# Kernel optimization log

Hardware: AMD Instinct MI355X
Metric: run time of the kernel (lower is better)

The kernel has to match this reference:

```python
import jax, jax.numpy as jnp
import numpy as np

N_NODES = 10000
N_EDGES = 160000
IN_DIM = 512
HID = 128
OUT = 64


def setup_inputs() -> dict:
    key = jax.random.key(0)
    ks = jax.random.split(key, 8)
    x = jax.random.normal(ks[0], (N_NODES, IN_DIM), dtype=jnp.float32)
    edge_index = jax.random.randint(ks[1], (2, N_EDGES), 0, N_NODES, dtype=jnp.int32)
    s = 0.02
    return {
        "x": x,
        "edge_index": edge_index,
        "W1_l": jax.random.normal(ks[2], (HID, IN_DIM), dtype=jnp.float32) * s,
        "W1_r": jax.random.normal(ks[3], (HID, IN_DIM), dtype=jnp.float32) * s,
        "b1": jnp.zeros((HID,), dtype=jnp.float32),
        "W2_l": jax.random.normal(ks[4], (OUT, HID), dtype=jnp.float32) * s,
        "W2_r": jax.random.normal(ks[5], (OUT, HID), dtype=jnp.float32) * s,
        "b2": jnp.zeros((OUT,), dtype=jnp.float32),
    }


def _sage_conv(x, src, dst, W_l, W_r, b, n_nodes):
    # PyG SAGEConv (aggr='mean', root_weight=True):
    #   out = lin_l(mean over incoming edges of x[src]) + lin_r(x)
    msg = x[src]  # [E, d] gather
    agg = jax.ops.segment_sum(msg, dst, num_segments=n_nodes)  # [N, d]
    cnt = jax.ops.segment_sum(jnp.ones_like(dst, dtype=x.dtype), dst, num_segments=n_nodes)
    agg = agg / jnp.maximum(cnt, 1.0)[:, None]  # mean with empty-node guard
    return agg @ W_l.T + x @ W_r.T + b


def reference(x, edge_index, W1_l, W1_r, b1, W2_l, W2_r, b2):
    src, dst = edge_index[0], edge_index[1]
    n = x.shape[0]
    h = _sage_conv(x, src, dst, W1_l, W1_r, b1, n)
    h = jax.nn.relu(h)
    z = _sage_conv(h, src, dst, W2_l, W2_r, b2, n)
    return z
```

## Files before the change

kernel.cpp:

```cpp
#include <hip/hip_runtime.h>

#define N_NODES 10000
#define N_EDGES 160000
#define IN_DIM 512
#define HID 128
#define OUT_DIM 64
#define CAP 64

typedef __attribute__((ext_vector_type(8))) short bf16x8;
typedef __attribute__((ext_vector_type(4))) float f32x4;

__device__ inline ushort f2b(float f) {
    unsigned u = __float_as_uint(f);
    u += 0x7fff + ((u >> 16) & 1);
    return (ushort)(u >> 16);
}
__device__ inline uint pack2(float a, float b) {
    return (uint)f2b(a) | ((uint)f2b(b) << 16);
}
__device__ inline float blo(uint u) { return __uint_as_float(u << 16); }
__device__ inline float bhi(uint u) { return __uint_as_float(u & 0xffff0000u); }

__global__ void zero_deg(int* __restrict__ deg) {
    int i = blockIdx.x * blockDim.x + threadIdx.x;
    if (i < N_NODES / 4) ((int4*)deg)[i] = make_int4(0, 0, 0, 0);
}

__device__ __forceinline__ void gemm1_body(int n0, int by,
    const float* __restrict__ A, const float* __restrict__ bpanel,
    ushort* __restrict__ XL, float* __restrict__ XR) {
    __shared__ __align__(16) ushort Asm[32 * 64];
    __shared__ __align__(16) ushort Bsm[64 * 64];

    const int t    = threadIdx.x;
    const int lane = t & 63;
    const int w    = t >> 6;
    const int wr   = w & 1;
    const int wc   = w >> 1;
    const int m0   = by * 32;
    const int kch  = lane >> 4;
    const int lrow = lane & 15;

    f32x4 acc[2] = {};

    for (int k0 = 0; k0 < IN_DIM; k0 += 64) {
        {
            int row = t >> 3, c = t & 7;
            int m = m0 + row;
            uint4 o = make_uint4(0u, 0u, 0u, 0u);
            if (m < N_NODES) {
                const float* p = A + (size_t)m * IN_DIM + k0 + c * 8;
                float4 v0 = reinterpret_cast<const float4*>(p)[0];
                float4 v1 = reinterpret_cast<const float4*>(p)[1];
                o.x = pack2(v0.x, v0.y); o.y = pack2(v0.z, v0.w);
                o.z = pack2(v1.x, v1.y); o.w = pack2(v1.z, v1.w);
            }
            *reinterpret_cast<uint4*>(&Asm[row * 64 + ((c ^ (row & 7)) << 3)]) = o;
        }
        #pragma unroll
        for (int ch = t; ch < 64 * 8; ch += 256) {
            int row = ch >> 3, c = ch & 7;
            const float* p = bpanel + (size_t)row * IN_DIM + k0 + c * 8;
            float4 v0 = reinterpret_cast<const float4*>(p)[0];
            float4 v1 = reinterpret_cast<const float4*>(p)[1];
            uint4 o;
            o.x = pack2(v0.x, v0.y); o.y = pack2(v0.z, v0.w);
            o.z = pack2(v1.x, v1.y); o.w = pack2(v1.z, v1.w);
            *reinterpret_cast<uint4*>(&Bsm[row * 64 + ((c ^ (row & 7)) << 3)]) = o;
        }
        __syncthreads();

        const int arow = wr * 16 + lrow;
        #pragma unroll
        for (int h = 0; h < 2; ++h) {
            int c = h * 4 + kch;
            bf16x8 afr = *reinterpret_cast<const bf16x8*>(&Asm[arow * 64 + ((c ^ (arow & 7)) << 3)]);
            #pragma unroll
            for (int cf = 0; cf < 2; ++cf) {
                int brow = wc * 32 + cf * 16 + lrow;
                bf16x8 bfr = *reinterpret_cast<const bf16x8*>(&Bsm[brow * 64 + ((c ^ (brow & 7)) << 3)]);
                acc[cf] = __builtin_amdgcn_mfma_f32_16x16x32_bf16(afr, bfr, acc[cf], 0, 0, 0);
            }
        }
        __syncthreads();
    }

    #pragma unroll
    for (int cf = 0; cf < 2; ++cf) {
        int col = n0 + wc * 32 + cf * 16 + lrow;
        #pragma unroll
        for (int j = 0; j < 4; ++j) {
            int row = m0 + wr * 16 + kch * 4 + j;
            if (row >= N_NODES) continue;
            if (col < HID) XL[(size_t)row * HID + col] = f2b(acc[cf][j]);
            else           XR[(size_t)row * HID + (col - HID)] = acc[cf][j];
        }
    }
}

#define ROWB ((N_NODES + 31) / 32)
#define G1_BLOCKS (4 * ROWB)
#define FILL_BLOCKS ((N_EDGES + 255) / 256)

__global__ __launch_bounds__(256) void fat_gemm1_fill(
    const float* __restrict__ x,
    const float* __restrict__ w1l, const float* __restrict__ w1r,
    ushort* __restrict__ XL, float* __restrict__ XR,
    const int* __restrict__ src, const int* __restrict__ dst,
    int* __restrict__ deg, int* __restrict__ bell) {
    int b = blockIdx.x;
    if (b < G1_BLOCKS) {
        int bx = b / ROWB, by = b % ROWB;
        const float* bpanel = (bx < 2) ? (w1l + (size_t)bx * 64 * IN_DIM)
                                       : (w1r + (size_t)(bx - 2) * 64 * IN_DIM);
        gemm1_body(bx * 64, by, x, bpanel, XL, XR);
    } else {
        int e = (b - G1_BLOCKS) * 256 + threadIdx.x;
        if (e < N_EDGES) {
            int d = dst[e];
            int pos = atomicAdd(&deg[d], 1);
            if (pos < CAP) bell[d * CAP + pos] = src[e];
        }
    }
}

__global__ __launch_bounds__(512) void gather1_gemm2(
    const ushort* __restrict__ XL, const float* __restrict__ XR,
    const float* __restrict__ b1, const int* __restrict__ deg,
    const int* __restrict__ bell,
    const float* __restrict__ w2l, const float* __restrict__ w2r,
    ushort* __restrict__ HL, float* __restrict__ HR) {
    __shared__ __align__(16) ushort Ah[32 * 128];
    __shared__ __align__(16) ushort Bs[128 * 128];

    const int t    = threadIdx.x;
    const int lane = t & 63;
    const int w    = t >> 6;
    const int base = blockIdx.x * 32;

    #pragma unroll
    for (int ch = t; ch < 128 * 16; ch += 512) {
        int row = ch >> 4, c = ch & 15;
        const float* p = ((row < 64) ? (w2l + (size_t)row * HID)
                                     : (w2r + (size_t)(row - 64) * HID)) + c * 8;
        float4 v0 = reinterpret_cast<const float4*>(p)[0];
        float4 v1 = reinterpret_cast<const float4*>(p)[1];
        uint4 o;
        o.x = pack2(v0.x, v0.y); o.y = pack2(v0.z, v0.w);
        o.z = pack2(v1.x, v1.y); o.w = pack2(v1.z, v1.w);
        *reinterpret_cast<uint4*>(&Bs[row * 128 + ((c ^ (row & 7)) << 3)]) = o;
    }

    #pragma unroll
    for (int q = 0; q < 4; ++q) {
        int r = w * 4 + q;
        int n = base + r;
        float v0 = 0.f, v1 = 0.f;
        if (n < N_NODES) {
            int d = min(deg[n], CAP);
            const int* lst = bell + (size_t)n * CAP;
            float a0 = 0.f, a1 = 0.f;
            int i = 0;
            for (; i + 4 <= d; i += 4) {
                int s0 = lst[i], s1 = lst[i + 1], s2 = lst[i + 2], s3 = lst[i + 3];
                uint u0 = *(const uint*)(XL + (size_t)s0 * 128 + lane * 2);
                uint u1 = *(const uint*)(XL + (size_t)s1 * 128 + lane * 2);
                uint u2 = *(const uint*)(XL + (size_t)s2 * 128 + lane * 2);
                uint u3 = *(const uint*)(XL + (size_t)s3 * 128 + lane * 2);
                a0 += blo(u0) + blo(u1) + blo(u2) + blo(u3);
                a1 += bhi(u0) + bhi(u1) + bhi(u2) + bhi(u3);
            }
            for (; i < d; ++i) {
                uint u = *(const uint*)(XL + (size_t)lst[i] * 128 + lane * 2);
                a0 += blo(u); a1 += bhi(u);
            }
            float inv = (d > 0) ? (1.0f / (float)d) : 0.0f;
            float2 xv = *(const float2*)&XR[(size_t)n * 128 + lane * 2];
            v0 = fmaxf(a0 * inv + xv.x + b1[lane * 2], 0.f);
            v1 = fmaxf(a1 * inv + xv.y + b1[lane * 2 + 1], 0.f);
        }
        int c = lane >> 2;
        *(uint*)&Ah[r * 128 + ((c ^ (r & 7)) << 3) + (lane & 3) * 2] = pack2(v0, v1);
    }
    __syncthreads();

    const int wr = w & 1, cw = w >> 1;
    const int kch = lane >> 4, lrow = lane & 15;
    const int arow = wr * 16 + lrow;
    f32x4 acc[2] = {};
    #pragma unroll
    for (int ks = 0; ks < 4; ++ks) {
        int c = ks * 4 + kch;
        bf16x8 afr = *reinterpret_cast<const bf16x8*>(&Ah[arow * 128 + ((c ^ (arow & 7)) << 3)]);
        #pragma unroll
        for (int cf = 0; cf < 2; ++cf) {
            int brow = cw * 32 + cf * 16 + lrow;
            bf16x8 bfr = *reinterpret_cast<const bf16x8*>(&Bs[brow * 128 + ((c ^ (brow & 7)) << 3)]);
            acc[cf] = __builtin_amdgcn_mfma_f32_16x16x32_bf16(afr, bfr, acc[cf], 0, 0, 0);
        }
    }

    #pragma unroll
    for (int cf = 0; cf < 2; ++cf) {
        int col = cw * 32 + cf * 16 + lrow;
        #pragma unroll
        for (int j = 0; j < 4; ++j) {
            int row = base + wr * 16 + kch * 4 + j;
            if (row >= N_NODES) continue;
            if (col < OUT_DIM) HL[(size_t)row * OUT_DIM + col] = f2b(acc[cf][j]);
            else               HR[(size_t)row * OUT_DIM + (col - OUT_DIM)] = acc[cf][j];
        }
    }
}

__global__ __launch_bounds__(256) void gather2(
    const ushort* __restrict__ V, const float* __restrict__ xr,
    const float* __restrict__ b, const int* __restrict__ deg,
    const int* __restrict__ bell, float* __restrict__ out) {
    int wave = threadIdx.x >> 6;
    int lane = threadIdx.x & 63;
    int n = blockIdx.x * 4 + wave;
    if (n >= N_NODES) return;

    int d = min(deg[n], CAP);
    const int* lst = bell + (size_t)n * CAP;

    float a0 = 0.f;
    int i = 0;
    for (; i + 4 <= d; i += 4) {
        int s0 = lst[i], s1 = lst[i + 1], s2 = lst[i + 2], s3 = lst[i + 3];
        a0 += blo((uint)V[(size_t)s0 * 64 + lane]) + blo((uint)V[(size_t)s1 * 64 + lane])
            + blo((uint)V[(size_t)s2 * 64 + lane]) + blo((uint)V[(size_t)s3 * 64 + lane]);
    }
    for (; i < d; ++i) a0 += blo((uint)V[(size_t)lst[i] * 64 + lane]);

    float inv = (d > 0) ? (1.0f / (float)d) : 0.0f;
    out[(size_t)n * 64 + lane] = a0 * inv + xr[(size_t)n * 64 + lane] + b[lane];
}

extern "C" void kernel_launch(void* const* d_in, const int* in_sizes, int n_in,
                              void* d_out, int out_size, void* d_ws, size_t ws_size,
                              hipStream_t stream) {
    const float* x   = (const float*)d_in[0];
    const int*   ei  = (const int*)d_in[1];
    const int*   src = ei;
    const int*   dst = ei + N_EDGES;
    const float* W1l = (const float*)d_in[2];
    const float* W1r = (const float*)d_in[3];
    const float* b1  = (const float*)d_in[4];
    const float* W2l = (const float*)d_in[5];
    const float* W2r = (const float*)d_in[6];
    const float* b2  = (const float*)d_in[7];
    float*       out = (float*)d_out;

    int* deg  = (int*)d_ws;
    int* bell = deg + N_NODES;
    ushort* XL = (ushort*)(bell + (size_t)N_NODES * CAP);
    float*  XR = (float*)(XL + (size_t)N_NODES * HID);
    ushort* HL = (ushort*)(XR + (size_t)N_NODES * HID);
    float*  HR = (float*)(HL + (size_t)N_NODES * OUT_DIM);

    zero_deg<<<(N_NODES / 4 + 255) / 256, 256, 0, stream>>>(deg);

    fat_gemm1_fill<<<G1_BLOCKS + FILL_BLOCKS, 256, 0, stream>>>(
        x, W1l, W1r, XL, XR, src, dst, deg, bell);

    gather1_gemm2<<<ROWB, 512, 0, stream>>>(XL, XR, b1, deg, bell, W2l, W2r, HL, HR);

    gather2<<<(N_NODES + 3) / 4, 256, 0, stream>>>(HL, HR, b2, deg, bell, out);
}
```

Measured before the change: 68.94 us.

## Widen GEMM1 tiles, store root terms in bf16, shrink gather1 blocks

GEMM1 blocks now compute 128 output columns instead of 64, which halves the GEMM1 grid and the number of times each x tile is re-read and converted. The root-weight intermediates XR and HR are stored as bf16 instead of fp32, halving their write and read traffic. The gather1+GEMM2 kernel moves to 16-row blocks of 1024 threads with one node per wave and one MFMA column tile per wave, which gives more blocks for the gather. This adds bf16 rounding on the root path, and each of the smaller gather1 blocks reloads the full W2 panel.

```diff
diff --git a/kernel.cpp b/kernel.cpp
--- a/kernel.cpp
+++ b/kernel.cpp
@@ -26,11 +26,12 @@
     if (i < N_NODES / 4) ((int4*)deg)[i] = make_int4(0, 0, 0, 0);
 }
 
-__device__ __forceinline__ void gemm1_body(int n0, int by,
+__device__ __forceinline__ void gemm1_body(int bx, int by,
     const float* __restrict__ A, const float* __restrict__ bpanel,
-    ushort* __restrict__ XL, float* __restrict__ XR) {
+    ushort* __restrict__ XL, ushort* __restrict__ XR) {
+    constexpr int CF = 4;
     __shared__ __align__(16) ushort Asm[32 * 64];
-    __shared__ __align__(16) ushort Bsm[64 * 64];
+    __shared__ __align__(16) ushort Bsm[128 * 64];
 
     const int t    = threadIdx.x;
     const int lane = t & 63;
@@ -38,10 +39,11 @@
     const int wr   = w & 1;
     const int wc   = w >> 1;
     const int m0   = by * 32;
+    const int n0   = bx * 128;
     const int kch  = lane >> 4;
     const int lrow = lane & 15;
 
-    f32x4 acc[2] = {};
+    f32x4 acc[CF] = {};
 
     for (int k0 = 0; k0 < IN_DIM; k0 += 64) {
         {
@@ -58,7 +60,7 @@
             *reinterpret_cast<uint4*>(&Asm[row * 64 + ((c ^ (row & 7)) << 3)]) = o;
         }
         #pragma unroll
-        for (int ch = t; ch < 64 * 8; ch += 256) {
+        for (int ch = t; ch < 128 * 8; ch += 256) {
             int row = ch >> 3, c = ch & 7;
             const float* p = bpanel + (size_t)row * IN_DIM + k0 + c * 8;
             float4 v0 = reinterpret_cast<const float4*>(p)[0];
@@ -76,8 +78,8 @@
             int c = h * 4 + kch;
             bf16x8 afr = *reinterpret_cast<const bf16x8*>(&Asm[arow * 64 + ((c ^ (arow & 7)) << 3)]);
             #pragma unroll
-            for (int cf = 0; cf < 2; ++cf) {
-                int brow = wc * 32 + cf * 16 + lrow;
+            for (int cf = 0; cf < CF; ++cf) {
+                int brow = wc * 64 + cf * 16 + lrow;
                 bf16x8 bfr = *reinterpret_cast<const bf16x8*>(&Bsm[brow * 64 + ((c ^ (brow & 7)) << 3)]);
                 acc[cf] = __builtin_amdgcn_mfma_f32_16x16x32_bf16(afr, bfr, acc[cf], 0, 0, 0);
             }
@@ -86,34 +88,32 @@
     }
 
     #pragma unroll
-    for (int cf = 0; cf < 2; ++cf) {
-        int col = n0 + wc * 32 + cf * 16 + lrow;
+    for (int cf = 0; cf < CF; ++cf) {
+        int col = n0 + wc * 64 + cf * 16 + lrow;
         #pragma unroll
         for (int j = 0; j < 4; ++j) {
             int row = m0 + wr * 16 + kch * 4 + j;
             if (row >= N_NODES) continue;
             if (col < HID) XL[(size_t)row * HID + col] = f2b(acc[cf][j]);
-            else           XR[(size_t)row * HID + (col - HID)] = acc[cf][j];
+            else           XR[(size_t)row * HID + (col - HID)] = f2b(acc[cf][j]);
         }
     }
 }
 
 #define ROWB ((N_NODES + 31) / 32)
-#define G1_BLOCKS (4 * ROWB)
+#define G1_BLOCKS (2 * ROWB)
 #define FILL_BLOCKS ((N_EDGES + 255) / 256)
 
 __global__ __launch_bounds__(256) void fat_gemm1_fill(
     const float* __restrict__ x,
     const float* __restrict__ w1l, const float* __restrict__ w1r,
-    ushort* __restrict__ XL, float* __restrict__ XR,
+    ushort* __restrict__ XL, ushort* __restrict__ XR,
     const int* __restrict__ src, const int* __restrict__ dst,
     int* __restrict__ deg, int* __restrict__ bell) {
     int b = blockIdx.x;
     if (b < G1_BLOCKS) {
         int bx = b / ROWB, by = b % ROWB;
-        const float* bpanel = (bx < 2) ? (w1l + (size_t)bx * 64 * IN_DIM)
-                                       : (w1r + (size_t)(bx - 2) * 64 * IN_DIM);
-        gemm1_body(bx * 64, by, x, bpanel, XL, XR);
+        gemm1_body(bx, by, x, (bx == 0) ? w1l : w1r, XL, XR);
     } else {
         int e = (b - G1_BLOCKS) * 256 + threadIdx.x;
         if (e < N_EDGES) {
@@ -124,22 +124,22 @@
     }
 }
 
-__global__ __launch_bounds__(512) void gather1_gemm2(
-    const ushort* __restrict__ XL, const float* __restrict__ XR,
+__global__ __launch_bounds__(1024) void gather1_gemm2(
+    const ushort* __restrict__ XL, const ushort* __restrict__ XR,
     const float* __restrict__ b1, const int* __restrict__ deg,
     const int* __restrict__ bell,
     const float* __restrict__ w2l, const float* __restrict__ w2r,
-    ushort* __restrict__ HL, float* __restrict__ HR) {
-    __shared__ __align__(16) ushort Ah[32 * 128];
+    ushort* __restrict__ HL, ushort* __restrict__ HR) {
+    __shared__ __align__(16) ushort Ah[16 * 128];
     __shared__ __align__(16) ushort Bs[128 * 128];
 
     const int t    = threadIdx.x;
     const int lane = t & 63;
     const int w    = t >> 6;
-    const int base = blockIdx.x * 32;
+    const int base = blockIdx.x * 16;
 
     #pragma unroll
-    for (int ch = t; ch < 128 * 16; ch += 512) {
+    for (int ch = t; ch < 128 * 16; ch += 1024) {
         int row = ch >> 4, c = ch & 15;
         const float* p = ((row < 64) ? (w2l + (size_t)row * HID)
                                      : (w2r + (size_t)(row - 64) * HID)) + c * 8;
@@ -151,10 +151,8 @@
         *reinterpret_cast<uint4*>(&Bs[row * 128 + ((c ^ (row & 7)) << 3)]) = o;
     }
 
-    #pragma unroll
-    for (int q = 0; q < 4; ++q) {
-        int r = w * 4 + q;
-        int n = base + r;
+    {
+        int n = base + w;
         float v0 = 0.f, v1 = 0.f;
         if (n < N_NODES) {
             int d = min(deg[n], CAP);
@@ -175,46 +173,40 @@
                 a0 += blo(u); a1 += bhi(u);
             }
             float inv = (d > 0) ? (1.0f / (float)d) : 0.0f;
-            float2 xv = *(const float2*)&XR[(size_t)n * 128 + lane * 2];
-            v0 = fmaxf(a0 * inv + xv.x + b1[lane * 2], 0.f);
-            v1 = fmaxf(a1 * inv + xv.y + b1[lane * 2 + 1], 0.f);
+            uint ux = *(const uint*)(XR + (size_t)n * 128 + lane * 2);
+            v0 = fmaxf(a0 * inv + blo(ux) + b1[lane * 2], 0.f);
+            v1 = fmaxf(a1 * inv + bhi(ux) + b1[lane * 2 + 1], 0.f);
         }
         int c = lane >> 2;
-        *(uint*)&Ah[r * 128 + ((c ^ (r & 7)) << 3) + (lane & 3) * 2] = pack2(v0, v1);
+        *(uint*)&Ah[w * 128 + ((c ^ (w & 7)) << 3) + (lane & 3) * 2] = pack2(v0, v1);
     }
     __syncthreads();
 
-    const int wr = w & 1, cw = w >> 1;
-    const int kch = lane >> 4, lrow = lane & 15;
-    const int arow = wr * 16 + lrow;
-    f32x4 acc[2] = {};
-    #pragma unroll
-    for (int ks = 0; ks < 4; ++ks) {
-        int c = ks * 4 + kch;
-        bf16x8 afr = *reinterpret_cast<const bf16x8*>(&Ah[arow * 128 + ((c ^ (arow & 7)) << 3)]);
-        #pragma unroll
-        for (int cf = 0; cf < 2; ++cf) {
-            int brow = cw * 32 + cf * 16 + lrow;
+    if (w < 8) {
+        const int kch = lane >> 4, lrow = lane & 15;
+        const int arow = lrow;
+        f32x4 acc = {};
+        #pragma unroll
+        for (int ks = 0; ks < 4; ++ks) {
+            int c = ks * 4 + kch;
+            bf16x8 afr = *reinterpret_cast<const bf16x8*>(&Ah[arow * 128 + ((c ^ (arow & 7)) << 3)]);
+            int brow = w * 16 + lrow;
             bf16x8 bfr = *reinterpret_cast<const bf16x8*>(&Bs[brow * 128 + ((c ^ (brow & 7)) << 3)]);
-            acc[cf] = __builtin_amdgcn_mfma_f32_16x16x32_bf16(afr, bfr, acc[cf], 0, 0, 0);
-        }
-    }
-
-    #pragma unroll
-    for (int cf = 0; cf < 2; ++cf) {
-        int col = cw * 32 + cf * 16 + lrow;
+            acc = __builtin_amdgcn_mfma_f32_16x16x32_bf16(afr, bfr, acc, 0, 0, 0);
+        }
+        int col = w * 16 + lrow;
         #pragma unroll
         for (int j = 0; j < 4; ++j) {
-            int row = base + wr * 16 + kch * 4 + j;
+            int row = base + kch * 4 + j;
             if (row >= N_NODES) continue;
-            if (col < OUT_DIM) HL[(size_t)row * OUT_DIM + col] = f2b(acc[cf][j]);
-            else               HR[(size_t)row * OUT_DIM + (col - OUT_DIM)] = acc[cf][j];
+            if (col < OUT_DIM) HL[(size_t)row * OUT_DIM + col] = f2b(acc[j]);
+            else               HR[(size_t)row * OUT_DIM + (col - OUT_DIM)] = f2b(acc[j]);
         }
     }
 }
 
 __global__ __launch_bounds__(256) void gather2(
-    const ushort* __restrict__ V, const float* __restrict__ xr,
+    const ushort* __restrict__ V, const ushort* __restrict__ xr,
     const float* __restrict__ b, const int* __restrict__ deg,
     const int* __restrict__ bell, float* __restrict__ out) {
     int wave = threadIdx.x >> 6;
@@ -235,7 +227,7 @@
     for (; i < d; ++i) a0 += blo((uint)V[(size_t)lst[i] * 64 + lane]);
 
     float inv = (d > 0) ? (1.0f / (float)d) : 0.0f;
-    out[(size_t)n * 64 + lane] = a0 * inv + xr[(size_t)n * 64 + lane] + b[lane];
+    out[(size_t)n * 64 + lane] = a0 * inv + blo((uint)xr[(size_t)n * 64 + lane]) + b[lane];
 }
 
 extern "C" void kernel_launch(void* const* d_in, const int* in_sizes, int n_in,
@@ -256,16 +248,17 @@
     int* deg  = (int*)d_ws;
     int* bell = deg + N_NODES;
     ushort* XL = (ushort*)(bell + (size_t)N_NODES * CAP);
-    float*  XR = (float*)(XL + (size_t)N_NODES * HID);
-    ushort* HL = (ushort*)(XR + (size_t)N_NODES * HID);
-    float*  HR = (float*)(HL + (size_t)N_NODES * OUT_DIM);
+    ushort* XR = XL + (size_t)N_NODES * HID;
+    ushort* HL = XR + (size_t)N_NODES * HID;
+    ushort* HR = HL + (size_t)N_NODES * OUT_DIM;
 
     zero_deg<<<(N_NODES / 4 + 255) / 256, 256, 0, stream>>>(deg);
 
     fat_gemm1_fill<<<G1_BLOCKS + FILL_BLOCKS, 256, 0, stream>>>(
         x, W1l, W1r, XL, XR, src, dst, deg, bell);
 
-    gather1_gemm2<<<ROWB, 512, 0, stream>>>(XL, XR, b1, deg, bell, W2l, W2r, HL, HR);
+    gather1_gemm2<<<(N_NODES + 15) / 16, 1024, 0, stream>>>(
+        XL, XR, b1, deg, bell, W2l, W2r, HL, HR);
 
     gather2<<<(N_NODES + 3) / 4, 256, 0, stream>>>(HL, HR, b2, deg, bell, out);
 }
```

After: 64.57 us. 6.3% less time.
